# Kernel tuning notes

Hardware: AMD Instinct MI355X
Metric: run time of the kernel (lower is better)

Reference implementation:

```python
import jax, jax.numpy as jnp
import numpy as np

H = 16          # query heads
KV = 8          # kv heads
D = 256         # head_dim
HID = 3584      # hidden_size
ROPE_BASE = 10000.0
SCALING = 256.0 ** -0.5          # query_pre_attn_scalar ** -0.5
SOFTCAP = 50.0                   # attn_logit_softcapping
WINDOW = 1536 - 1                # sliding_window - 1 (layer_idx 0 is even)


def _rope_neox(x, positions):
    # x: [T, nh, D]; neox style: rotate the two halves of the head dim
    half = D // 2
    inv_freq = 1.0 / (ROPE_BASE ** (jnp.arange(0, D, 2, dtype=jnp.float32) / D))  # [half]
    freqs = positions.astype(jnp.float32)[:, None] * inv_freq[None, :]            # [T, half]
    cos = jnp.cos(freqs)[:, None, :]  # [T, 1, half]
    sin = jnp.sin(freqs)[:, None, :]
    x1, x2 = x[..., :half], x[..., half:]
    return jnp.concatenate([x1 * cos - x2 * sin, x2 * cos + x1 * sin], axis=-1)


def setup_inputs() -> dict:
    key = jax.random.key(0)
    k1, k2, k3 = jax.random.split(key, 3)
    T = 3072
    hidden_states = jax.random.normal(k1, (T, HID), dtype=jnp.float32)
    w_qkv = jax.random.normal(k2, (H * D + 2 * KV * D, HID), dtype=jnp.float32) * 0.02
    w_o = jax.random.normal(k3, (HID, H * D), dtype=jnp.float32) * 0.02
    positions = jnp.arange(T, dtype=jnp.int64)
    return {"positions": positions, "hidden_states": hidden_states,
            "w_qkv": w_qkv, "w_o": w_o}


def reference(positions, hidden_states, w_qkv, w_o):
    T = hidden_states.shape[0]
    qkv = hidden_states @ w_qkv.T                       # [T, (H+2KV)*D]
    q, k, v = jnp.split(qkv, [H * D, H * D + KV * D], axis=-1)
    q = q.reshape(T, H, D)
    k = k.reshape(T, KV, D)
    v = v.reshape(T, KV, D)
    q = _rope_neox(q, positions)
    k = _rope_neox(k, positions)
    # GQA: repeat kv heads (2 query heads per kv head)
    k = jnp.repeat(k, H // KV, axis=1)                  # [T, H, D]
    v = jnp.repeat(v, H // KV, axis=1)
    scores = jnp.einsum('thd,shd->hts', q, k) * SCALING  # [H, T, T]
    scores = SOFTCAP * jnp.tanh(scores / SOFTCAP)       # logit softcapping
    i = positions[:, None]
    j = positions[None, :]
    mask = (j <= i) & (i - j <= WINDOW)                 # causal + sliding window
    scores = jnp.where(mask[None, :, :], scores, -jnp.inf)
    probs = jax.nn.softmax(scores, axis=-1)
    attn = jnp.einsum('hts,shd->thd', probs, v).reshape(T, H * D)
    return attn @ w_o.T                                 # [T, HID]
```

## Files before the change

kernel.cpp:

```cpp
#include <hip/hip_runtime.h>
#include <math.h>

typedef unsigned short u16;
typedef __attribute__((ext_vector_type(8))) short short8;
typedef __attribute__((ext_vector_type(4))) float f32x4;
typedef __attribute__((ext_vector_type(4))) unsigned short u16x4;

#define HN 16
#define KVH 8
#define DH 256
#define HID 3584
#define T_LEN 3072
#define QKV_N 8192
#define O_N 4096
#define WIN 1535
#define SCALING 0.0625f
#define SOFTCAP 50.0f
#define KOFF 4096
#define VOFF 6144
#define PSTR 72
#define NJT 48
#define M_FIX 20.0f

__device__ __forceinline__ u16 f2bf(float f) {
  unsigned u = __float_as_uint(f);
  u += 0x7FFFu + ((u >> 16) & 1u);
  return (u16)(u >> 16);
}
__device__ __forceinline__ float bf2f(u16 b) {
  return __uint_as_float(((unsigned)b) << 16);
}

__device__ __forceinline__ void gload_lds16(const void* g, void* l) {
  __builtin_amdgcn_global_load_lds(
      (const __attribute__((address_space(1))) void*)g,
      (__attribute__((address_space(3))) void*)l, 16, 0, 0);
}

__device__ __forceinline__ f32x4 mfma_bf16(short8 a, short8 b, f32x4 c) {
  return __builtin_amdgcn_mfma_f32_16x16x32_bf16(a, b, c, 0, 0, 0);
}

#define BARX()                                  \
  do {                                          \
    __builtin_amdgcn_sched_barrier(0);          \
    __builtin_amdgcn_s_barrier();               \
    __builtin_amdgcn_sched_barrier(0);          \
  } while (0)

__global__ __launch_bounds__(256) void cvt2_kernel(const float* __restrict__ a,
                                                   u16* __restrict__ da, int nva,
                                                   const float* __restrict__ b,
                                                   u16* __restrict__ db, int nvb,
                                                   float* __restrict__ rtab) {
  const int bid = blockIdx.x;
  if (bid < 1536) {
    int idx = bid * 256 + threadIdx.x;
    int d = idx & 127;
    int t = idx >> 7;
    float inv = exp2f((float)d * (-13.287712379549449f / 128.0f));
    float ang = (float)t * inv;
    float2 cs;
    cs.x = cosf(ang);
    cs.y = sinf(ang);
    *(float2*)(rtab + (size_t)idx * 2) = cs;
  }
  int v = bid * 256 + threadIdx.x;
  const float* src;
  u16* dst;
  if (v < nva) {
    src = a + (size_t)v * 4;
    dst = da + (size_t)v * 4;
  } else if (v < nva + nvb) {
    int u = v - nva;
    src = b + (size_t)u * 4;
    dst = db + (size_t)u * 4;
  } else {
    return;
  }
  float4 x = *(const float4*)src;
  u16x4 o;
  o[0] = f2bf(x.x); o[1] = f2bf(x.y); o[2] = f2bf(x.z); o[3] = f2bf(x.w);
  *(u16x4*)dst = o;
}

__global__ __launch_bounds__(512, 2) void gemm1_kernel(const u16* __restrict__ A,
                                                       const u16* __restrict__ B,
                                                       u16* __restrict__ C,
                                                       const float* __restrict__ rtab) {
  __shared__ u16 sA[2][256 * 64];
  __shared__ u16 sB[2][256 * 64];

  const int N = QKV_N, K = HID;
  const int bid = blockIdx.x;
  const int tid = threadIdx.x;
  const int lane = tid & 63, wid = tid >> 6;
  const int NT = K >> 6;
  const int srow = lane >> 3;
  const int sg = (lane & 7) ^ srow;
  const int fr = lane & 15;
  const int fh = fr & 7;
  const int gk0 = (lane >> 4) ^ fh;
  const int gk1 = ((lane >> 4) + 4) ^ fh;

  int bm, bn, row0, mhalf = 0;
  const int isFull = (bid < 256);
  if (isFull) {
    const int wg = (bid & 7) * 32 + (bid >> 3);
    bm = wg >> 5; bn = wg & 31;
    row0 = bm * 256;
  } else {
    const int j = bid - 256;
    mhalf = j >> 7;
    const int j2 = j & 127;
    const int s = (j2 & 7) * 16 + (j2 >> 3);
    bm = 8 + (s >> 5); bn = s & 31;
    row0 = bm * 256 + mhalf * 128;
  }
  const int col0 = bn * 256;
  const int wc = wid & 3;

  auto stage = [&](int tau, int kind) {
    if (tau >= NT) return;
    const int b = tau & 1;
    const u16* src;
    u16* dst;
    if (kind >= 2) {
      const int rbase = (kind - 2) * 128;
      src = A + (size_t)(row0 + rbase + wid * 8 + srow) * K + (size_t)tau * 64 + sg * 8;
      dst = &sA[b][(rbase + wid * 8) * 64];
    } else {
      const int rbase = kind * 128;
      src = B + (size_t)(col0 + rbase + wid * 8 + srow) * K + (size_t)tau * 64 + sg * 8;
      dst = &sB[b][(rbase + wid * 8) * 64];
    }
    gload_lds16(src, dst);
    gload_lds16(src + (size_t)64 * K, dst + 64 * 64);
  };

#define CMAP(ni) (wc * 32 + ((ni) & 1) * 16 + ((ni) >> 1) * 128)
#define LDB_(pB, ni, kk) (*(const short8*)&pB[(CMAP(ni) + fr) * 64 + (kk ? gk1 : gk0) * 8])
#define LDA_(pA, mrow, kk) (*(const short8*)&pA[((mrow) + fr) * 64 + (kk ? gk1 : gk0) * 8])
#define MFMA2(AF, acc0, acc1)                                            \
  __builtin_amdgcn_s_setprio(1);                                        \
  _Pragma("unroll") for (int ni = 0; ni < 4; ++ni) {                    \
    acc0[ni] = mfma_bf16(AF[0][0], bf[ni][0], acc0[ni]);                \
    acc0[ni] = mfma_bf16(AF[0][1], bf[ni][1], acc0[ni]);                \
    acc1[ni] = mfma_bf16(AF[1][0], bf[ni][0], acc1[ni]);                \
    acc1[ni] = mfma_bf16(AF[1][1], bf[ni][1], acc1[ni]);                \
  }                                                                      \
  __builtin_amdgcn_s_setprio(0);                                        \
  asm volatile("s_waitcnt lgkmcnt(0)" ::: "memory");

#define ROPE_WRITE(ACC, MROWG)                                           \
  _Pragma("unroll") for (int nh = 0; nh < 2; ++nh) {                    \
    const int dlo = wc * 32 + nh * 16 + fr;                             \
    _Pragma("unroll") for (int j = 0; j < 4; ++j) {                     \
      const int r = (MROWG) + (lane >> 4) * 4 + j;                      \
      float2 cs = *(const float2*)(rtab + ((size_t)(r << 7) + dlo) * 2);\
      float xlo = ACC[nh][j], xhi = ACC[nh + 2][j];                     \
      C[(size_t)r * N + col0 + dlo] = f2bf(xlo * cs.x - xhi * cs.y);    \
      C[(size_t)r * N + col0 + dlo + 128] = f2bf(xhi * cs.x + xlo * cs.y); \
    }                                                                    \
  }
#define PLAIN_WRITE(ACC, MROWG)                                          \
  _Pragma("unroll") for (int ni = 0; ni < 4; ++ni) {                    \
    const int r0 = (MROWG) + (lane >> 4) * 4;                           \
    const int c = col0 + CMAP(ni) + fr;                                 \
    _Pragma("unroll") for (int j = 0; j < 4; ++j)                       \
      C[(size_t)(r0 + j) * N + c] = f2bf(ACC[ni][j]);                   \
  }

  if (isFull) {
    const int wr = wid >> 2;
    f32x4 acc[8][4] = {};
    stage(0, 0); stage(0, 1); stage(0, 2); stage(0, 3);
    stage(1, 0); stage(1, 1); stage(1, 2);
    __builtin_amdgcn_sched_barrier(0);
    asm volatile("s_waitcnt vmcnt(6)" ::: "memory");
    BARX();

    for (int u = 0; u < NT; ++u) {
      const int b = u & 1;
      const u16* pA = &sA[b][0];
      const u16* pB = &sB[b][0];
      short8 bf[4][2], afA[2][2], afB[2][2];
#pragma unroll
      for (int ni = 0; ni < 4; ++ni) { bf[ni][0] = LDB_(pB, ni, 0); bf[ni][1] = LDB_(pB, ni, 1); }
      afA[0][0] = LDA_(pA, wr * 128 + 0 * 16, 0); afA[0][1] = LDA_(pA, wr * 128 + 0 * 16, 1);
      afA[1][0] = LDA_(pA, wr * 128 + 1 * 16, 0); afA[1][1] = LDA_(pA, wr * 128 + 1 * 16, 1);
      stage(u + 1, 3);
      BARX();
      MFMA2(afA, acc[0], acc[1]);
      BARX();
      afA[0][0] = LDA_(pA, wr * 128 + 2 * 16, 0); afA[0][1] = LDA_(pA, wr * 128 + 2 * 16, 1);
      afA[1][0] = LDA_(pA, wr * 128 + 3 * 16, 0); afA[1][1] = LDA_(pA, wr * 128 + 3 * 16, 1);
      stage(u + 2, 0);
      BARX();
      MFMA2(afA, acc[2], acc[3]);
      BARX();
      afA[0][0] = LDA_(pA, wr * 128 + 4 * 16, 0); afA[0][1] = LDA_(pA, wr * 128 + 4 * 16, 1);
      afA[1][0] = LDA_(pA, wr * 128 + 5 * 16, 0); afA[1][1] = LDA_(pA, wr * 128 + 5 * 16, 1);
      afB[0][0] = LDA_(pA, wr * 128 + 6 * 16, 0); afB[0][1] = LDA_(pA, wr * 128 + 6 * 16, 1);
      afB[1][0] = LDA_(pA, wr * 128 + 7 * 16, 0); afB[1][1] = LDA_(pA, wr * 128 + 7 * 16, 1);
      stage(u + 2, 1);
      BARX();
      MFMA2(afA, acc[4], acc[5]);
      BARX();
      stage(u + 2, 2);
      __builtin_amdgcn_sched_barrier(0);
      if (u + 2 < NT) {
        asm volatile("s_waitcnt vmcnt(6)" ::: "memory");
      } else {
        asm volatile("s_waitcnt vmcnt(0)" ::: "memory");
      }
      BARX();
      MFMA2(afB, acc[6], acc[7]);
      BARX();
    }
    if (bn < 24) {
#pragma unroll
      for (int mi = 0; mi < 8; ++mi) { ROPE_WRITE(acc[mi], row0 + wr * 128 + mi * 16); }
    } else {
#pragma unroll
      for (int mi = 0; mi < 8; ++mi) { PLAIN_WRITE(acc[mi], row0 + wr * 128 + mi * 16); }
    }
  } else {
    const int wr = wid >> 2;
    f32x4 acc[4][4] = {};
    stage(0, 0); stage(0, 1); stage(0, 2);
    stage(1, 0); stage(1, 1);
    __builtin_amdgcn_sched_barrier(0);
    asm volatile("s_waitcnt vmcnt(4)" ::: "memory");
    BARX();

    for (int u = 0; u < NT; ++u) {
      const int b = u & 1;
      const u16* pA = &sA[b][0];
      const u16* pB = &sB[b][0];
      short8 bf[4][2], afA[2][2], afB[2][2];
#pragma unroll
      for (int ni = 0; ni < 4; ++ni) { bf[ni][0] = LDB_(pB, ni, 0); bf[ni][1] = LDB_(pB, ni, 1); }
      afA[0][0] = LDA_(pA, wr * 64 + 0 * 16, 0); afA[0][1] = LDA_(pA, wr * 64 + 0 * 16, 1);
      afA[1][0] = LDA_(pA, wr * 64 + 1 * 16, 0); afA[1][1] = LDA_(pA, wr * 64 + 1 * 16, 1);
      stage(u + 1, 2);
      BARX();
      MFMA2(afA, acc[0], acc[1]);
      BARX();
      afB[0][0] = LDA_(pA, wr * 64 + 2 * 16, 0); afB[0][1] = LDA_(pA, wr * 64 + 2 * 16, 1);
      afB[1][0] = LDA_(pA, wr * 64 + 3 * 16, 0); afB[1][1] = LDA_(pA, wr * 64 + 3 * 16, 1);
      stage(u + 2, 0); stage(u + 2, 1);
      __builtin_amdgcn_sched_barrier(0);
      if (u + 2 < NT) {
        asm volatile("s_waitcnt vmcnt(4)" ::: "memory");
      } else {
        asm volatile("s_waitcnt vmcnt(0)" ::: "memory");
      }
      BARX();
      MFMA2(afB, acc[2], acc[3]);
      BARX();
    }
    if (bn < 24) {
#pragma unroll
      for (int mi = 0; mi < 4; ++mi) { ROPE_WRITE(acc[mi], row0 + wr * 64 + mi * 16); }
    } else {
#pragma unroll
      for (int mi = 0; mi < 4; ++mi) { PLAIN_WRITE(acc[mi], row0 + wr * 64 + mi * 16); }
    }
  }
#undef CMAP
#undef LDB_
#undef LDA_
#undef MFMA2
#undef ROPE_WRITE
#undef PLAIN_WRITE
}

__global__ __launch_bounds__(512, 2) void gemm8p(const u16* __restrict__ A,
                                                 const u16* __restrict__ B,
                                                 float* __restrict__ C,
                                                 int N, int K, int ntn, int cpx) {
  __shared__ u16 sA[2][256 * 64];
  __shared__ u16 sB[2][256 * 64];

  const int bid = blockIdx.x;
  const int tid = threadIdx.x;
  const int wg = (bid & 7) * cpx + (bid >> 3);
  const int bm = wg / ntn, bn = wg % ntn;
  const int row0 = bm * 256, col0 = bn * 256;
  const int lane = tid & 63, wid = tid >> 6;
  const int wr = wid >> 2, wc = wid & 3;
  const int NT = K >> 6;

  const int srow = lane >> 3;
  const int sg = (lane & 7) ^ srow;

  auto stage = [&](int tau, int kind) {
    if (tau >= NT) return;
    const int b = tau & 1;
    const int rbase = (kind & 1) * 128;
    const u16* src;
    u16* dst;
    if (kind >= 2) {
      src = A + (size_t)(row0 + rbase + wid * 8 + srow) * K + (size_t)tau * 64 + sg * 8;
      dst = &sA[b][(rbase + wid * 8) * 64];
    } else {
      src = B + (size_t)(col0 + rbase + wid * 8 + srow) * K + (size_t)tau * 64 + sg * 8;
      dst = &sB[b][(rbase + wid * 8) * 64];
    }
    gload_lds16(src, dst);
    gload_lds16(src + (size_t)64 * K, dst + 64 * 64);
  };

  f32x4 acc[8][4] = {};
  const int fr = lane & 15;
  const int fh = fr & 7;
  const int gk0 = (lane >> 4) ^ fh;
  const int gk1 = ((lane >> 4) + 4) ^ fh;

  stage(0, 0); stage(0, 1); stage(0, 2); stage(0, 3);
  stage(1, 0); stage(1, 1); stage(1, 2);
  __builtin_amdgcn_sched_barrier(0);
  asm volatile("s_waitcnt vmcnt(6)" ::: "memory");
  BARX();

  for (int u = 0; u < NT; ++u) {
    const int b = u & 1;
    const u16* pA = &sA[b][0];
    const u16* pB = &sB[b][0];
    short8 bf[4][2], afA[2][2], afB[2][2];

#define CMAP(ni) (wc * 32 + ((ni) & 1) * 16 + ((ni) >> 1) * 128)
#define LDB_(ni, kk) (*(const short8*)&pB[(CMAP(ni) + fr) * 64 + (kk ? gk1 : gk0) * 8])
#define LDA_(mi, kk) (*(const short8*)&pA[(wr * 128 + (mi)*16 + fr) * 64 + (kk ? gk1 : gk0) * 8])
#define MFMA2(AF, mi0)                                                   \
  __builtin_amdgcn_s_setprio(1);                                        \
  _Pragma("unroll") for (int ni = 0; ni < 4; ++ni) {                    \
    acc[mi0][ni] = mfma_bf16(AF[0][0], bf[ni][0], acc[mi0][ni]);        \
    acc[mi0][ni] = mfma_bf16(AF[0][1], bf[ni][1], acc[mi0][ni]);        \
    acc[mi0 + 1][ni] = mfma_bf16(AF[1][0], bf[ni][0], acc[mi0 + 1][ni]);\
    acc[mi0 + 1][ni] = mfma_bf16(AF[1][1], bf[ni][1], acc[mi0 + 1][ni]);\
  }                                                                      \
  __builtin_amdgcn_s_setprio(0);                                        \
  asm volatile("s_waitcnt lgkmcnt(0)" ::: "memory");

#pragma unroll
    for (int ni = 0; ni < 4; ++ni) { bf[ni][0] = LDB_(ni, 0); bf[ni][1] = LDB_(ni, 1); }
    afA[0][0] = LDA_(0, 0); afA[0][1] = LDA_(0, 1);
    afA[1][0] = LDA_(1, 0); afA[1][1] = LDA_(1, 1);
    stage(u + 1, 3);
    BARX();
    MFMA2(afA, 0);
    BARX();
    afA[0][0] = LDA_(2, 0); afA[0][1] = LDA_(2, 1);
    afA[1][0] = LDA_(3, 0); afA[1][1] = LDA_(3, 1);
    stage(u + 2, 0);
    BARX();
    MFMA2(afA, 2);
    BARX();
    afA[0][0] = LDA_(4, 0); afA[0][1] = LDA_(4, 1);
    afA[1][0] = LDA_(5, 0); afA[1][1] = LDA_(5, 1);
    afB[0][0] = LDA_(6, 0); afB[0][1] = LDA_(6, 1);
    afB[1][0] = LDA_(7, 0); afB[1][1] = LDA_(7, 1);
    stage(u + 2, 1);
    BARX();
    MFMA2(afA, 4);
    BARX();
    stage(u + 2, 2);
    __builtin_amdgcn_sched_barrier(0);
    if (u + 2 < NT) {
      asm volatile("s_waitcnt vmcnt(6)" ::: "memory");
    } else {
      asm volatile("s_waitcnt vmcnt(0)" ::: "memory");
    }
    BARX();
    MFMA2(afB, 6);
    BARX();
#undef CMAP
#undef LDB_
#undef LDA_
#undef MFMA2
  }

#pragma unroll
  for (int mi = 0; mi < 8; ++mi) {
#pragma unroll
    for (int ni = 0; ni < 4; ++ni) {
      const int r = row0 + wr * 128 + mi * 16 + (lane >> 4) * 4;
      const int c = col0 + wc * 32 + (ni & 1) * 16 + (ni >> 1) * 128 + fr;
#pragma unroll
      for (int j = 0; j < 4; ++j)
        C[(size_t)(r + j) * N + c] = acc[mi][ni][j];
    }
  }
}

__global__ __launch_bounds__(256) void vtrans_kernel(const u16* __restrict__ qkv,
                                                     u16* __restrict__ vt) {
  __shared__ u16 tile[256 * 72];
  const int jb = blockIdx.x * 64;
  const int kvh = blockIdx.y;
  const int tid = threadIdx.x;
  const int t = tid & 63, dc = tid >> 6;

  const u16* src = qkv + (size_t)(jb + t) * QKV_N + VOFF + kvh * DH + dc * 64;
#pragma unroll
  for (int i = 0; i < 8; ++i) {
    short8 v = *(const short8*)(src + i * 8);
    int d0 = dc * 64 + i * 8;
#pragma unroll
    for (int j = 0; j < 8; ++j) tile[(d0 + j) * 72 + t] = (u16)(short)v[j];
  }
  __syncthreads();

  u16* dst = vt + ((size_t)kvh * NJT + blockIdx.x) * 16384;
#pragma unroll
  for (int s = 0; s < 8; ++s) {
    int G = s * 256 + tid;
    int d = G >> 3, g = G & 7;
    short8 x = *(const short8*)&tile[d * 72 + ((g ^ (d & 7)) * 8)];
    *(short8*)(dst + G * 8) = x;
  }
}

__global__ __launch_bounds__(256) void attn_kernel(const u16* __restrict__ qkv,
                                                   const u16* __restrict__ vt,
                                                   u16* __restrict__ po,
                                                   float* __restrict__ ml) {
  const int wg = blockIdx.x;
  const int kvh = wg & 7;
  const int rest = wg >> 3;
  const int qt = rest >> 2;
  const int c = (rest >> 1) & 1;
  const int h = kvh * 2 + (rest & 1);
  const int qb = qt * 64;
  const int tid = threadIdx.x, lane = tid & 63, w = tid >> 6;

  __shared__ u16 sK[64 * 256];
  __shared__ u16 sVt[64 * 256];
  __shared__ u16 sP[4][16 * PSTR];

  int jmin = qb - WIN; if (jmin < 0) jmin = 0;
  const int jt0 = jmin >> 6, jt1 = qb >> 6;
  const int nt = jt1 - jt0 + 1;
  const int half = (nt + 1) >> 1;
  const int t_beg = (c == 0) ? jt0 : jt0 + half;
  const int t_end = (c == 0) ? jt0 + half : jt1 + 1;

  const int qrow = qb + w * 16 + (lane & 15);
  short8 qf[8];
  {
    const u16* qp = qkv + (size_t)qrow * QKV_N + h * DH + (lane >> 4) * 8;
#pragma unroll
    for (int kc = 0; kc < 8; ++kc) qf[kc] = *(const short8*)(qp + kc * 32);
  }

  f32x4 O[16];
#pragma unroll
  for (int i = 0; i < 16; ++i) O[i] = f32x4{0.f, 0.f, 0.f, 0.f};
  float lrow[4] = {0.f, 0.f, 0.f, 0.f};

  const int dl = lane & 15;
  const int vb0 = dl * 64 + (((lane >> 4)) ^ (dl & 7)) * 8;
  const int vb1 = dl * 64 + (((lane >> 4) + 4) ^ (dl & 7)) * 8;

  for (int jt = t_beg; jt < t_end; ++jt) {
    const int jb = jt * 64;
#pragma unroll
    for (int i = 0; i < 8; ++i) {
      int rl = w * 16 + i * 2 + (lane >> 5);
      int g = (lane & 31) ^ (rl & 7);
      gload_lds16(qkv + (size_t)(jb + rl) * QKV_N + KOFF + kvh * DH + g * 8,
                  &sK[(w * 16 + i * 2) * 256]);
    }
    {
      const u16* vtile = vt + ((size_t)kvh * NJT + jt) * 16384;
#pragma unroll
      for (int s = 0; s < 8; ++s) {
        int id = w * 8 + s;
        gload_lds16(vtile + id * 512 + lane * 8, &sVt[id * 512]);
      }
    }
    __syncthreads();

    f32x4 S[4];
#pragma unroll
    for (int nf = 0; nf < 4; ++nf) S[nf] = f32x4{0.f, 0.f, 0.f, 0.f};
#pragma unroll
    for (int nf = 0; nf < 4; ++nf) {
      int krow = nf * 16 + (lane & 15);
#pragma unroll
      for (int kc = 0; kc < 8; ++kc) {
        int g = (kc * 4 + (lane >> 4)) ^ (krow & 7);
        short8 kf = *(const short8*)&sK[krow * 256 + g * 8];
        S[nf] = mfma_bf16(qf[kc], kf, S[nf]);
      }
    }

#pragma unroll
    for (int r = 0; r < 4; ++r) {
      const int irow = qb + w * 16 + (lane >> 4) * 4 + r;
      const int ql = (lane >> 4) * 4 + r;
#pragma unroll
      for (int nf = 0; nf < 4; ++nf) {
        int j = jb + nf * 16 + (lane & 15);
        float x = S[nf][r] * (SCALING / SOFTCAP);
        float e2 = __expf(-2.0f * fabsf(x));
        float th = (1.0f - e2) / (1.0f + e2);
        th = x >= 0.0f ? th : -th;
        float val = SOFTCAP * th;
        bool ok = (j <= irow) && (irow - j <= WIN);
        float p = ok ? __expf(val - M_FIX) : 0.0f;
        lrow[r] += p;
        sP[w][ql * PSTR + nf * 16 + (lane & 15)] = f2bf(p);
      }
    }

    short8 pf0 = *(const short8*)&sP[w][(lane & 15) * PSTR + (lane >> 4) * 8];
    short8 pf1 = *(const short8*)&sP[w][(lane & 15) * PSTR + 32 + (lane >> 4) * 8];
#pragma unroll
    for (int nf = 0; nf < 16; ++nf) {
      short8 vf0 = *(const short8*)&sVt[nf * 1024 + vb0];
      short8 vf1 = *(const short8*)&sVt[nf * 1024 + vb1];
      O[nf] = mfma_bf16(pf0, vf0, O[nf]);
      O[nf] = mfma_bf16(pf1, vf1, O[nf]);
    }
    __syncthreads();
  }

#pragma unroll
  for (int r = 0; r < 4; ++r) {
#pragma unroll
    for (int off = 8; off >= 1; off >>= 1) lrow[r] += __shfl_xor(lrow[r], off);
  }

#pragma unroll
  for (int nf = 0; nf < 16; ++nf) {
    int d = nf * 16 + (lane & 15);
#pragma unroll
    for (int r = 0; r < 4; ++r) {
      int trow = qb + w * 16 + (lane >> 4) * 4 + r;
      po[(((size_t)c * T_LEN + trow) * HN + h) * DH + d] = f2bf(O[nf][r]);
    }
  }
  if ((lane & 15) == 0) {
#pragma unroll
    for (int r = 0; r < 4; ++r) {
      int trow = qb + w * 16 + (lane >> 4) * 4 + r;
      size_t mi = (((size_t)c * T_LEN + trow) * HN + h) * 2;
      ml[mi] = M_FIX;
      ml[mi + 1] = lrow[r];
    }
  }
}

__global__ __launch_bounds__(256) void combine_kernel(const u16* __restrict__ po,
                                                      const float* __restrict__ ml,
                                                      u16* __restrict__ attnb,
                                                      const float* __restrict__ wo,
                                                      u16* __restrict__ wob) {
  const int t = blockIdx.x;
  const int h = threadIdx.x >> 4;
  const int d0 = (threadIdx.x & 15) * 16;
  const size_t row = (size_t)t * HN + h;
  const float l0 = ml[row * 2 + 1];
  const float l1 = ml[(size_t)T_LEN * HN * 2 + row * 2 + 1];
  const float inv = 1.0f / (l0 + l1);
  const size_t i0 = row * DH + d0;
  const size_t i1 = (size_t)T_LEN * HN * DH + i0;
#pragma unroll
  for (int half = 0; half < 2; ++half) {
    short8 x0 = *(const short8*)(po + i0 + half * 8);
    short8 x1 = *(const short8*)(po + i1 + half * 8);
    short8 o;
#pragma unroll
    for (int j = 0; j < 8; ++j)
      o[j] = (short)f2bf((bf2f((u16)x0[j]) + bf2f((u16)x1[j])) * inv);
    *(short8*)(attnb + i0 + half * 8) = o;
  }

  const int nv = (HID * O_N) / 4;
  for (int v = blockIdx.x * 256 + threadIdx.x; v < nv; v += T_LEN * 256) {
    float4 x = *(const float4*)(wo + (size_t)v * 4);
    u16x4 o;
    o[0] = f2bf(x.x); o[1] = f2bf(x.y); o[2] = f2bf(x.z); o[3] = f2bf(x.w);
    *(u16x4*)(wob + (size_t)v * 4) = o;
  }
}

extern "C" void kernel_launch(void* const* d_in, const int* in_sizes, int n_in,
                              void* d_out, int out_size, void* d_ws, size_t ws_size,
                              hipStream_t stream) {
  const float* hidden = (const float*)d_in[1];
  const float* w_qkv = (const float*)d_in[2];
  const float* w_o = (const float*)d_in[3];
  float* out = (float*)d_out;
  char* ws = (char*)d_ws;

  u16* wqkvb = (u16*)(ws);
  u16* po = (u16*)(ws);
  float* ml = (float*)(ws + 50331648);
  u16* attnb = (u16*)(ws);
  u16* hb = (u16*)(ws + 58720256);
  u16* vtb = (u16*)(ws + 58720256);
  u16* qkvb = (u16*)(ws + 80740352);
  u16* wob = (u16*)(ws + 80740352);
  float* ropetab = out;

  {
    int nva = T_LEN * HID / 4;
    int nvb = QKV_N * HID / 4;
    cvt2_kernel<<<dim3((nva + nvb + 255) / 256), 256, 0, stream>>>(
        hidden, hb, nva, w_qkv, wqkvb, nvb, ropetab);
  }
  gemm1_kernel<<<dim3(512), 512, 0, stream>>>(hb, wqkvb, qkvb, ropetab);
  vtrans_kernel<<<dim3(NJT, KVH), 256, 0, stream>>>(qkvb, vtb);
  attn_kernel<<<dim3(1536), 256, 0, stream>>>(qkvb, vtb, po, ml);
  combine_kernel<<<dim3(T_LEN), 256, 0, stream>>>(po, ml, attnb, w_o, wob);
  gemm8p<<<dim3(168), 512, 0, stream>>>(attnb, wob, out, HID, O_N, 14, 21);
}
```

Measured before the change: 541.0 us.

## Use split-K with atomic accumulation for QKV GEMM tail tiles and separate RoPE kernel

The QKV GEMM's tail row block (rows 2048-3071) previously used half-height 128-row tiles to fill the grid. It now uses full 256x256 tiles split along K into two halves, which accumulate via float atomics into a zeroed scratch buffer inside the output allocation. RoPE is moved out of the GEMM epilogue into a separate rope_kernel, which also converts the scratch V region to bf16. The intent is to balance the waves and keep the larger, more efficient tile shape everywhere. In exchange it adds a memset, atomic traffic, an extra kernel launch, and a second read and write pass over Q/K for RoPE.

```diff
diff --git a/kernel.cpp b/kernel.cpp
--- a/kernel.cpp
+++ b/kernel.cpp
@@ -87,7 +87,7 @@
 __global__ __launch_bounds__(512, 2) void gemm1_kernel(const u16* __restrict__ A,
                                                        const u16* __restrict__ B,
                                                        u16* __restrict__ C,
-                                                       const float* __restrict__ rtab) {
+                                                       float* __restrict__ scratch) {
   __shared__ u16 sA[2][256 * 64];
   __shared__ u16 sB[2][256 * 64];
 
@@ -95,7 +95,7 @@
   const int bid = blockIdx.x;
   const int tid = threadIdx.x;
   const int lane = tid & 63, wid = tid >> 6;
-  const int NT = K >> 6;
+  const int wr = wid >> 2, wc = wid & 3;
   const int srow = lane >> 3;
   const int sg = (lane & 7) ^ srow;
   const int fr = lane & 15;
@@ -103,177 +103,165 @@
   const int gk0 = (lane >> 4) ^ fh;
   const int gk1 = ((lane >> 4) + 4) ^ fh;
 
-  int bm, bn, row0, mhalf = 0;
+  int bm, bn, kbase, NTL;
   const int isFull = (bid < 256);
   if (isFull) {
     const int wg = (bid & 7) * 32 + (bid >> 3);
     bm = wg >> 5; bn = wg & 31;
-    row0 = bm * 256;
+    kbase = 0; NTL = 56;
   } else {
     const int j = bid - 256;
-    mhalf = j >> 7;
-    const int j2 = j & 127;
-    const int s = (j2 & 7) * 16 + (j2 >> 3);
-    bm = 8 + (s >> 5); bn = s & 31;
-    row0 = bm * 256 + mhalf * 128;
-  }
-  const int col0 = bn * 256;
-  const int wc = wid & 3;
+    const int t = j >> 1;
+    const int half = j & 1;
+    const int wgt = (t & 7) * 16 + (t >> 3);
+    bm = 8 + (wgt >> 5); bn = wgt & 31;
+    kbase = half * 28; NTL = 28;
+  }
+  const int row0 = bm * 256, col0 = bn * 256;
 
   auto stage = [&](int tau, int kind) {
-    if (tau >= NT) return;
+    if (tau >= NTL) return;
     const int b = tau & 1;
+    const int rbase = (kind & 1) * 128;
     const u16* src;
     u16* dst;
     if (kind >= 2) {
-      const int rbase = (kind - 2) * 128;
-      src = A + (size_t)(row0 + rbase + wid * 8 + srow) * K + (size_t)tau * 64 + sg * 8;
+      src = A + (size_t)(row0 + rbase + wid * 8 + srow) * K +
+            (size_t)(kbase + tau) * 64 + sg * 8;
       dst = &sA[b][(rbase + wid * 8) * 64];
     } else {
-      const int rbase = kind * 128;
-      src = B + (size_t)(col0 + rbase + wid * 8 + srow) * K + (size_t)tau * 64 + sg * 8;
+      src = B + (size_t)(col0 + rbase + wid * 8 + srow) * K +
+            (size_t)(kbase + tau) * 64 + sg * 8;
       dst = &sB[b][(rbase + wid * 8) * 64];
     }
     gload_lds16(src, dst);
     gload_lds16(src + (size_t)64 * K, dst + 64 * 64);
   };
 
-#define CMAP(ni) (wc * 32 + ((ni) & 1) * 16 + ((ni) >> 1) * 128)
-#define LDB_(pB, ni, kk) (*(const short8*)&pB[(CMAP(ni) + fr) * 64 + (kk ? gk1 : gk0) * 8])
-#define LDA_(pA, mrow, kk) (*(const short8*)&pA[((mrow) + fr) * 64 + (kk ? gk1 : gk0) * 8])
-#define MFMA2(AF, acc0, acc1)                                            \
+  f32x4 acc[8][4] = {};
+
+  stage(0, 0); stage(0, 1); stage(0, 2); stage(0, 3);
+  stage(1, 0); stage(1, 1); stage(1, 2);
+  __builtin_amdgcn_sched_barrier(0);
+  asm volatile("s_waitcnt vmcnt(6)" ::: "memory");
+  BARX();
+
+  for (int u = 0; u < NTL; ++u) {
+    const int b = u & 1;
+    const u16* pA = &sA[b][0];
+    const u16* pB = &sB[b][0];
+    short8 bf[4][2], afA[2][2], afB[2][2];
+
+#define LDB_(ni, kk) (*(const short8*)&pB[(wc * 64 + (ni)*16 + fr) * 64 + (kk ? gk1 : gk0) * 8])
+#define LDA_(mi, kk) (*(const short8*)&pA[(wr * 128 + (mi)*16 + fr) * 64 + (kk ? gk1 : gk0) * 8])
+#define MFMA2(AF, mi0)                                                   \
   __builtin_amdgcn_s_setprio(1);                                        \
   _Pragma("unroll") for (int ni = 0; ni < 4; ++ni) {                    \
-    acc0[ni] = mfma_bf16(AF[0][0], bf[ni][0], acc0[ni]);                \
-    acc0[ni] = mfma_bf16(AF[0][1], bf[ni][1], acc0[ni]);                \
-    acc1[ni] = mfma_bf16(AF[1][0], bf[ni][0], acc1[ni]);                \
-    acc1[ni] = mfma_bf16(AF[1][1], bf[ni][1], acc1[ni]);                \
+    acc[mi0][ni] = mfma_bf16(AF[0][0], bf[ni][0], acc[mi0][ni]);        \
+    acc[mi0][ni] = mfma_bf16(AF[0][1], bf[ni][1], acc[mi0][ni]);        \
+    acc[mi0 + 1][ni] = mfma_bf16(AF[1][0], bf[ni][0], acc[mi0 + 1][ni]);\
+    acc[mi0 + 1][ni] = mfma_bf16(AF[1][1], bf[ni][1], acc[mi0 + 1][ni]);\
   }                                                                      \
   __builtin_amdgcn_s_setprio(0);                                        \
   asm volatile("s_waitcnt lgkmcnt(0)" ::: "memory");
 
-#define ROPE_WRITE(ACC, MROWG)                                           \
-  _Pragma("unroll") for (int nh = 0; nh < 2; ++nh) {                    \
-    const int dlo = wc * 32 + nh * 16 + fr;                             \
-    _Pragma("unroll") for (int j = 0; j < 4; ++j) {                     \
-      const int r = (MROWG) + (lane >> 4) * 4 + j;                      \
-      float2 cs = *(const float2*)(rtab + ((size_t)(r << 7) + dlo) * 2);\
-      float xlo = ACC[nh][j], xhi = ACC[nh + 2][j];                     \
-      C[(size_t)r * N + col0 + dlo] = f2bf(xlo * cs.x - xhi * cs.y);    \
-      C[(size_t)r * N + col0 + dlo + 128] = f2bf(xhi * cs.x + xlo * cs.y); \
-    }                                                                    \
-  }
-#define PLAIN_WRITE(ACC, MROWG)                                          \
-  _Pragma("unroll") for (int ni = 0; ni < 4; ++ni) {                    \
-    const int r0 = (MROWG) + (lane >> 4) * 4;                           \
-    const int c = col0 + CMAP(ni) + fr;                                 \
-    _Pragma("unroll") for (int j = 0; j < 4; ++j)                       \
-      C[(size_t)(r0 + j) * N + c] = f2bf(ACC[ni][j]);                   \
-  }
-
-  if (isFull) {
-    const int wr = wid >> 2;
-    f32x4 acc[8][4] = {};
-    stage(0, 0); stage(0, 1); stage(0, 2); stage(0, 3);
-    stage(1, 0); stage(1, 1); stage(1, 2);
+#pragma unroll
+    for (int ni = 0; ni < 4; ++ni) { bf[ni][0] = LDB_(ni, 0); bf[ni][1] = LDB_(ni, 1); }
+    afA[0][0] = LDA_(0, 0); afA[0][1] = LDA_(0, 1);
+    afA[1][0] = LDA_(1, 0); afA[1][1] = LDA_(1, 1);
+    stage(u + 1, 3);
+    BARX();
+    MFMA2(afA, 0);
+    BARX();
+    afA[0][0] = LDA_(2, 0); afA[0][1] = LDA_(2, 1);
+    afA[1][0] = LDA_(3, 0); afA[1][1] = LDA_(3, 1);
+    stage(u + 2, 0);
+    BARX();
+    MFMA2(afA, 2);
+    BARX();
+    afA[0][0] = LDA_(4, 0); afA[0][1] = LDA_(4, 1);
+    afA[1][0] = LDA_(5, 0); afA[1][1] = LDA_(5, 1);
+    afB[0][0] = LDA_(6, 0); afB[0][1] = LDA_(6, 1);
+    afB[1][0] = LDA_(7, 0); afB[1][1] = LDA_(7, 1);
+    stage(u + 2, 1);
+    BARX();
+    MFMA2(afA, 4);
+    BARX();
+    stage(u + 2, 2);
     __builtin_amdgcn_sched_barrier(0);
-    asm volatile("s_waitcnt vmcnt(6)" ::: "memory");
-    BARX();
-
-    for (int u = 0; u < NT; ++u) {
-      const int b = u & 1;
-      const u16* pA = &sA[b][0];
-      const u16* pB = &sB[b][0];
-      short8 bf[4][2], afA[2][2], afB[2][2];
-#pragma unroll
-      for (int ni = 0; ni < 4; ++ni) { bf[ni][0] = LDB_(pB, ni, 0); bf[ni][1] = LDB_(pB, ni, 1); }
-      afA[0][0] = LDA_(pA, wr * 128 + 0 * 16, 0); afA[0][1] = LDA_(pA, wr * 128 + 0 * 16, 1);
-      afA[1][0] = LDA_(pA, wr * 128 + 1 * 16, 0); afA[1][1] = LDA_(pA, wr * 128 + 1 * 16, 1);
-      stage(u + 1, 3);
-      BARX();
-      MFMA2(afA, acc[0], acc[1]);
-      BARX();
-      afA[0][0] = LDA_(pA, wr * 128 + 2 * 16, 0); afA[0][1] = LDA_(pA, wr * 128 + 2 * 16, 1);
-      afA[1][0] = LDA_(pA, wr * 128 + 3 * 16, 0); afA[1][1] = LDA_(pA, wr * 128 + 3 * 16, 1);
-      stage(u + 2, 0);
-      BARX();
-      MFMA2(afA, acc[2], acc[3]);
-      BARX();
-      afA[0][0] = LDA_(pA, wr * 128 + 4 * 16, 0); afA[0][1] = LDA_(pA, wr * 128 + 4 * 16, 1);
-      afA[1][0] = LDA_(pA, wr * 128 + 5 * 16, 0); afA[1][1] = LDA_(pA, wr * 128 + 5 * 16, 1);
-      afB[0][0] = LDA_(pA, wr * 128 + 6 * 16, 0); afB[0][1] = LDA_(pA, wr * 128 + 6 * 16, 1);
-      afB[1][0] = LDA_(pA, wr * 128 + 7 * 16, 0); afB[1][1] = LDA_(pA, wr * 128 + 7 * 16, 1);
-      stage(u + 2, 1);
-      BARX();
-      MFMA2(afA, acc[4], acc[5]);
-      BARX();
-      stage(u + 2, 2);
-      __builtin_amdgcn_sched_barrier(0);
-      if (u + 2 < NT) {
-        asm volatile("s_waitcnt vmcnt(6)" ::: "memory");
-      } else {
-        asm volatile("s_waitcnt vmcnt(0)" ::: "memory");
-      }
-      BARX();
-      MFMA2(afB, acc[6], acc[7]);
-      BARX();
-    }
-    if (bn < 24) {
-#pragma unroll
-      for (int mi = 0; mi < 8; ++mi) { ROPE_WRITE(acc[mi], row0 + wr * 128 + mi * 16); }
+    if (u + 2 < NTL) {
+      asm volatile("s_waitcnt vmcnt(6)" ::: "memory");
     } else {
-#pragma unroll
-      for (int mi = 0; mi < 8; ++mi) { PLAIN_WRITE(acc[mi], row0 + wr * 128 + mi * 16); }
-    }
-  } else {
-    const int wr = wid >> 2;
-    f32x4 acc[4][4] = {};
-    stage(0, 0); stage(0, 1); stage(0, 2);
-    stage(1, 0); stage(1, 1);
-    __builtin_amdgcn_sched_barrier(0);
-    asm volatile("s_waitcnt vmcnt(4)" ::: "memory");
-    BARX();
-
-    for (int u = 0; u < NT; ++u) {
-      const int b = u & 1;
-      const u16* pA = &sA[b][0];
-      const u16* pB = &sB[b][0];
-      short8 bf[4][2], afA[2][2], afB[2][2];
-#pragma unroll
-      for (int ni = 0; ni < 4; ++ni) { bf[ni][0] = LDB_(pB, ni, 0); bf[ni][1] = LDB_(pB, ni, 1); }
-      afA[0][0] = LDA_(pA, wr * 64 + 0 * 16, 0); afA[0][1] = LDA_(pA, wr * 64 + 0 * 16, 1);
-      afA[1][0] = LDA_(pA, wr * 64 + 1 * 16, 0); afA[1][1] = LDA_(pA, wr * 64 + 1 * 16, 1);
-      stage(u + 1, 2);
-      BARX();
-      MFMA2(afA, acc[0], acc[1]);
-      BARX();
-      afB[0][0] = LDA_(pA, wr * 64 + 2 * 16, 0); afB[0][1] = LDA_(pA, wr * 64 + 2 * 16, 1);
-      afB[1][0] = LDA_(pA, wr * 64 + 3 * 16, 0); afB[1][1] = LDA_(pA, wr * 64 + 3 * 16, 1);
-      stage(u + 2, 0); stage(u + 2, 1);
-      __builtin_amdgcn_sched_barrier(0);
-      if (u + 2 < NT) {
-        asm volatile("s_waitcnt vmcnt(4)" ::: "memory");
-      } else {
-        asm volatile("s_waitcnt vmcnt(0)" ::: "memory");
-      }
-      BARX();
-      MFMA2(afB, acc[2], acc[3]);
-      BARX();
-    }
-    if (bn < 24) {
-#pragma unroll
-      for (int mi = 0; mi < 4; ++mi) { ROPE_WRITE(acc[mi], row0 + wr * 64 + mi * 16); }
-    } else {
-#pragma unroll
-      for (int mi = 0; mi < 4; ++mi) { PLAIN_WRITE(acc[mi], row0 + wr * 64 + mi * 16); }
-    }
-  }
-#undef CMAP
+      asm volatile("s_waitcnt vmcnt(0)" ::: "memory");
+    }
+    BARX();
+    MFMA2(afB, 6);
+    BARX();
 #undef LDB_
 #undef LDA_
 #undef MFMA2
-#undef ROPE_WRITE
-#undef PLAIN_WRITE
+  }
+
+  if (isFull) {
+#pragma unroll
+    for (int mi = 0; mi < 8; ++mi) {
+#pragma unroll
+      for (int ni = 0; ni < 4; ++ni) {
+        const int r = row0 + wr * 128 + mi * 16 + (lane >> 4) * 4;
+        const int c = col0 + wc * 64 + ni * 16 + (lane & 15);
+#pragma unroll
+        for (int j = 0; j < 4; ++j)
+          C[(size_t)(r + j) * N + c] = f2bf(acc[mi][ni][j]);
+      }
+    }
+  } else {
+#pragma unroll
+    for (int mi = 0; mi < 8; ++mi) {
+#pragma unroll
+      for (int ni = 0; ni < 4; ++ni) {
+        const int r = row0 + wr * 128 + mi * 16 + (lane >> 4) * 4;
+        const int c = col0 + wc * 64 + ni * 16 + (lane & 15);
+#pragma unroll
+        for (int j = 0; j < 4; ++j)
+          unsafeAtomicAdd(&scratch[(size_t)(r + j - 2048) * N + c], acc[mi][ni][j]);
+      }
+    }
+  }
+}
+
+__global__ __launch_bounds__(256) void rope_kernel(u16* __restrict__ qkv,
+                                                   const float* __restrict__ tab,
+                                                   const float* __restrict__ scratch) {
+  const int idx = blockIdx.x * 256 + threadIdx.x;
+  const int d = idx & 127;
+  const int hh = (idx >> 7) % 24;
+  const int t = idx / (24 * 128);
+  if (t < T_LEN) {
+    const size_t coloff = (hh < HN ? hh * DH : HN * DH + (hh - HN) * DH);
+    float2 cs = *(const float2*)(tab + ((size_t)(t << 7) + d) * 2);
+    const size_t base = (size_t)t * QKV_N + coloff;
+    float x1, x2;
+    if (t < 2048) {
+      x1 = bf2f(qkv[base + d]);
+      x2 = bf2f(qkv[base + d + 128]);
+    } else {
+      const float* sp = scratch + (size_t)(t - 2048) * QKV_N + coloff;
+      x1 = sp[d];
+      x2 = sp[d + 128];
+    }
+    qkv[base + d] = f2bf(x1 * cs.x - x2 * cs.y);
+    qkv[base + d + 128] = f2bf(x2 * cs.x + x1 * cs.y);
+  }
+  const int NV4 = (1024 * 2048) / 4;
+  if (idx < NV4) {
+    const int row = idx >> 9;
+    const int c4 = idx & 511;
+    const size_t soff = (size_t)row * QKV_N + VOFF + (size_t)c4 * 4;
+    float4 x = *(const float4*)(scratch + soff);
+    u16x4 o;
+    o[0] = f2bf(x.x); o[1] = f2bf(x.y); o[2] = f2bf(x.z); o[3] = f2bf(x.w);
+    *(u16x4*)(qkv + (size_t)(2048 + row) * QKV_N + VOFF + (size_t)c4 * 4) = o;
+  }
 }
 
 __global__ __launch_bounds__(512, 2) void gemm8p(const u16* __restrict__ A,
@@ -330,8 +318,7 @@
     const u16* pB = &sB[b][0];
     short8 bf[4][2], afA[2][2], afB[2][2];
 
-#define CMAP(ni) (wc * 32 + ((ni) & 1) * 16 + ((ni) >> 1) * 128)
-#define LDB_(ni, kk) (*(const short8*)&pB[(CMAP(ni) + fr) * 64 + (kk ? gk1 : gk0) * 8])
+#define LDB_(ni, kk) (*(const short8*)&pB[(wc * 64 + (ni)*16 + fr) * 64 + (kk ? gk1 : gk0) * 8])
 #define LDA_(mi, kk) (*(const short8*)&pA[(wr * 128 + (mi)*16 + fr) * 64 + (kk ? gk1 : gk0) * 8])
 #define MFMA2(AF, mi0)                                                   \
   __builtin_amdgcn_s_setprio(1);                                        \
@@ -376,7 +363,6 @@
     BARX();
     MFMA2(afB, 6);
     BARX();
-#undef CMAP
 #undef LDB_
 #undef LDA_
 #undef MFMA2
@@ -387,7 +373,7 @@
 #pragma unroll
     for (int ni = 0; ni < 4; ++ni) {
       const int r = row0 + wr * 128 + mi * 16 + (lane >> 4) * 4;
-      const int c = col0 + wc * 32 + (ni & 1) * 16 + (ni >> 1) * 128 + fr;
+      const int c = col0 + wc * 64 + ni * 16 + (lane & 15);
 #pragma unroll
       for (int j = 0; j < 4; ++j)
         C[(size_t)(r + j) * N + c] = acc[mi][ni][j];
@@ -606,14 +592,20 @@
   u16* qkvb = (u16*)(ws + 80740352);
   u16* wob = (u16*)(ws + 80740352);
   float* ropetab = out;
-
+  float* kscratch = (float*)((char*)d_out + 4194304);
+
+  hipMemsetAsync(kscratch, 0, (size_t)1024 * QKV_N * 4, stream);
   {
     int nva = T_LEN * HID / 4;
     int nvb = QKV_N * HID / 4;
     cvt2_kernel<<<dim3((nva + nvb + 255) / 256), 256, 0, stream>>>(
         hidden, hb, nva, w_qkv, wqkvb, nvb, ropetab);
   }
-  gemm1_kernel<<<dim3(512), 512, 0, stream>>>(hb, wqkvb, qkvb, ropetab);
+  gemm1_kernel<<<dim3(512), 512, 0, stream>>>(hb, wqkvb, qkvb, kscratch);
+  {
+    int n = T_LEN * 24 * 128;
+    rope_kernel<<<dim3(n / 256), 256, 0, stream>>>(qkvb, ropetab, kscratch);
+  }
   vtrans_kernel<<<dim3(NJT, KVH), 256, 0, stream>>>(qkvb, vtb);
   attn_kernel<<<dim3(1536), 256, 0, stream>>>(qkvb, vtb, po, ml);
   combine_kernel<<<dim3(T_LEN), 256, 0, stream>>>(po, ml, attnb, w_o, wob);
```

Result: slower. 576.1 us (+6.5%).
